# Kernel tuning notes

Hardware: AMD Instinct MI355X
Metric: run time of the kernel (lower is better)

Reference implementation:

```python
import jax, jax.numpy as jnp
import numpy as np

N_NODES = 100000
N_EDGES = 1600000
D_FEAT = 64


def setup_inputs() -> dict:
    key = jax.random.key(0)
    k1, k2, k3 = jax.random.split(key, 3)
    x = jax.random.normal(k1, (N_NODES, D_FEAT), dtype=jnp.float32)
    edge_weight = jax.random.uniform(k2, (N_EDGES,), dtype=jnp.float32)
    edge_index = jax.random.randint(k3, (2, N_EDGES), 0, N_NODES, dtype=jnp.int64)
    return {"x": x, "edge_weight": edge_weight, "edge_index": edge_index}


def reference(x, edge_weight, edge_index):
    # GCNConv with lin.weight forced to identity, improved=False,
    # add_self_loops=True, normalize=True, bias=False.
    N = x.shape[0]
    row, col = edge_index[0], edge_index[1]  # source, target

    # add self loops with fill weight 1.0 (improved=False)
    loop = jnp.arange(N, dtype=edge_index.dtype)
    row = jnp.concatenate([row, loop])
    col = jnp.concatenate([col, loop])
    w = jnp.concatenate([edge_weight, jnp.ones((N,), dtype=x.dtype)])

    # symmetric GCN normalization: deg computed at target (col)
    deg = jax.ops.segment_sum(w, col, num_segments=N)
    deg_inv_sqrt = jnp.where(deg > 0, jax.lax.rsqrt(deg), 0.0)
    norm = deg_inv_sqrt[row] * w * deg_inv_sqrt[col]  # [E+N]

    # gather source features, weight, scatter-add to targets
    msg = x[row] * norm[:, None]                      # [E+N, F]
    out = jax.ops.segment_sum(msg, col, num_segments=N)
    return out
```

## Files before the change

### kernel.cpp

```cpp
#include <hip/hip_runtime.h>

constexpr int N_NODES  = 100000;
constexpr int N_EDGES  = 1600000;
constexpr int D_FEAT   = 64;
constexpr int SCAN_BLK = 1024;
constexpr int NB       = (N_NODES + SCAN_BLK - 1) / SCAN_BLK;

__global__ void k_zero(unsigned long long* __restrict__ packed) {
    int i = blockIdx.x * blockDim.x + threadIdx.x;
    if (i < N_NODES) packed[i] = 0ull;
}

__global__ void k_hist(const float* __restrict__ ew, const int* __restrict__ col,
                       unsigned long long* __restrict__ packed,
                       uchar4* __restrict__ rank4) {
    int t = blockIdx.x * blockDim.x + threadIdx.x;
    if (t >= N_EDGES / 4) return;
    const int4   c4 = ((const int4*)col)[t];
    const float4 w4 = ((const float4*)ew)[t];

    unsigned long long a0 = (1ull << 32) | (unsigned long long)(unsigned int)(w4.x * 16777216.0f + 0.5f);
    unsigned long long a1 = (1ull << 32) | (unsigned long long)(unsigned int)(w4.y * 16777216.0f + 0.5f);
    unsigned long long a2 = (1ull << 32) | (unsigned long long)(unsigned int)(w4.z * 16777216.0f + 0.5f);
    unsigned long long a3 = (1ull << 32) | (unsigned long long)(unsigned int)(w4.w * 16777216.0f + 0.5f);

    unsigned long long o0 = atomicAdd(&packed[c4.x], a0);
    unsigned long long o1 = atomicAdd(&packed[c4.y], a1);
    unsigned long long o2 = atomicAdd(&packed[c4.z], a2);
    unsigned long long o3 = atomicAdd(&packed[c4.w], a3);

    rank4[t] = make_uchar4((unsigned char)(o0 >> 32), (unsigned char)(o1 >> 32),
                           (unsigned char)(o2 >> 32), (unsigned char)(o3 >> 32));
}

__global__ void k_scan_a(const unsigned long long* __restrict__ packed,
                         float* __restrict__ dinv,
                         int* __restrict__ ptr, int* __restrict__ bsum) {
    __shared__ int s[SCAN_BLK];
    int tid = threadIdx.x;
    int gid = blockIdx.x * SCAN_BLK + tid;
    int v = 0;
    if (gid < N_NODES) {
        unsigned long long p = packed[gid];
        v = (int)(p >> 32);
        float deg = (float)(unsigned int)(p & 0xffffffffu) * (1.0f / 16777216.0f);
        dinv[gid] = rsqrtf(deg + 1.0f);
    }
    s[tid] = v;
    __syncthreads();
    for (int off = 1; off < SCAN_BLK; off <<= 1) {
        int t = (tid >= off) ? s[tid - off] : 0;
        __syncthreads();
        s[tid] += t;
        __syncthreads();
    }
    if (gid < N_NODES) ptr[gid] = s[tid] - v;
    if (tid == SCAN_BLK - 1) bsum[blockIdx.x] = s[tid];
}

__global__ void k_scan_b(const int* __restrict__ bsum, int* __restrict__ boff) {
    __shared__ int s[128];
    int tid = threadIdx.x;
    int v = (tid < NB) ? bsum[tid] : 0;
    s[tid] = v;
    __syncthreads();
    for (int off = 1; off < 128; off <<= 1) {
        int t = (tid >= off) ? s[tid - off] : 0;
        __syncthreads();
        s[tid] += t;
        __syncthreads();
    }
    if (tid < NB) boff[tid] = s[tid] - v;
}

__global__ void k_scan_c(const int* __restrict__ boff, int* __restrict__ ptr) {
    int gid = blockIdx.x * SCAN_BLK + threadIdx.x;
    if (gid < N_NODES) ptr[gid] += boff[blockIdx.x];
    if (gid == 0) ptr[N_NODES] = N_EDGES;
}

__global__ void k_scatter(const int* __restrict__ row, const int* __restrict__ col,
                          const float* __restrict__ ew, const float* __restrict__ dinv,
                          const uchar4* __restrict__ rank4,
                          const int* __restrict__ ptr, int2* __restrict__ csr) {
    int t = blockIdx.x * blockDim.x + threadIdx.x;
    if (t >= N_EDGES / 4) return;
    const int4   r4 = ((const int4*)row)[t];
    const int4   c4 = ((const int4*)col)[t];
    const float4 w4 = ((const float4*)ew)[t];
    const uchar4 k4 = rank4[t];

    float d0 = dinv[r4.x], d1 = dinv[r4.y], d2 = dinv[r4.z], d3 = dinv[r4.w];
    int p0 = ptr[c4.x] + k4.x;
    int p1 = ptr[c4.y] + k4.y;
    int p2 = ptr[c4.z] + k4.z;
    int p3 = ptr[c4.w] + k4.w;

    csr[p0] = make_int2(r4.x, __float_as_int(w4.x * d0));
    csr[p1] = make_int2(r4.y, __float_as_int(w4.y * d1));
    csr[p2] = make_int2(r4.z, __float_as_int(w4.z * d2));
    csr[p3] = make_int2(r4.w, __float_as_int(w4.w * d3));
}

__global__ void k_gather(const float* __restrict__ x, const float* __restrict__ dinv,
                         const int* __restrict__ ptr,
                         const int2* __restrict__ csr, float* __restrict__ out) {
    long long gid = (long long)blockIdx.x * blockDim.x + threadIdx.x;
    int node = (int)(gid >> 6);
    if (node >= N_NODES) return;
    int lane = (int)(gid & 63);
    int sub  = lane >> 4;
    int q    = lane & 15;

    int start = ptr[node];
    int n     = ptr[node + 1] - start;

    float4 acc = make_float4(0.f, 0.f, 0.f, 0.f);
    int k = sub;
    for (; k + 4 < n; k += 8) {
        int2 pa = csr[start + k];
        int2 pb = csr[start + k + 4];
        const float4 xa = ((const float4*)(x + (size_t)pa.x * D_FEAT))[q];
        const float4 xb = ((const float4*)(x + (size_t)pb.x * D_FEAT))[q];
        float sa = __int_as_float(pa.y);
        float sb = __int_as_float(pb.y);
        acc.x = fmaf(sa, xa.x, acc.x); acc.y = fmaf(sa, xa.y, acc.y);
        acc.z = fmaf(sa, xa.z, acc.z); acc.w = fmaf(sa, xa.w, acc.w);
        acc.x = fmaf(sb, xb.x, acc.x); acc.y = fmaf(sb, xb.y, acc.y);
        acc.z = fmaf(sb, xb.z, acc.z); acc.w = fmaf(sb, xb.w, acc.w);
    }
    if (k < n) {
        int2 p = csr[start + k];
        const float4 xv = ((const float4*)(x + (size_t)p.x * D_FEAT))[q];
        float s = __int_as_float(p.y);
        acc.x = fmaf(s, xv.x, acc.x); acc.y = fmaf(s, xv.y, acc.y);
        acc.z = fmaf(s, xv.z, acc.z); acc.w = fmaf(s, xv.w, acc.w);
    }

    acc.x += __shfl_xor(acc.x, 16); acc.x += __shfl_xor(acc.x, 32);
    acc.y += __shfl_xor(acc.y, 16); acc.y += __shfl_xor(acc.y, 32);
    acc.z += __shfl_xor(acc.z, 16); acc.z += __shfl_xor(acc.z, 32);
    acc.w += __shfl_xor(acc.w, 16); acc.w += __shfl_xor(acc.w, 32);

    if (sub == 0) {
        float di = dinv[node];
        const float4 xs = ((const float4*)(x + (size_t)node * D_FEAT))[q];
        float4 o;
        o.x = di * acc.x + di * di * xs.x;
        o.y = di * acc.y + di * di * xs.y;
        o.z = di * acc.z + di * di * xs.z;
        o.w = di * acc.w + di * di * xs.w;
        ((float4*)(out + (size_t)node * D_FEAT))[q] = o;
    }
}

extern "C" void kernel_launch(void* const* d_in, const int* in_sizes, int n_in,
                              void* d_out, int out_size, void* d_ws, size_t ws_size,
                              hipStream_t stream) {
    const float* x   = (const float*)d_in[0];
    const float* ew  = (const float*)d_in[1];
    const int*   ei  = (const int*)d_in[2];
    const int*   row = ei;
    const int*   col = ei + N_EDGES;
    float* out = (float*)d_out;

    char* ws = (char*)d_ws;
    unsigned long long* packed = (unsigned long long*)(ws);
    float*         dinv  = (float*)(ws + 800000);
    int*           ptr   = (int*)(ws + 1200000);
    int*           bsum  = (int*)(ws + 1600016);
    int*           boff  = (int*)(ws + 1600528);
    uchar4*        rank4 = (uchar4*)(ws + 1601040);
    int2*          csr   = (int2*)(ws + 3201040);

    const int B = 256;

    k_zero<<<(N_NODES + B - 1) / B, B, 0, stream>>>(packed);
    k_hist<<<(N_EDGES / 4 + B - 1) / B, B, 0, stream>>>(ew, col, packed, rank4);
    k_scan_a<<<NB, SCAN_BLK, 0, stream>>>(packed, dinv, ptr, bsum);
    k_scan_b<<<1, 128, 0, stream>>>(bsum, boff);
    k_scan_c<<<NB, SCAN_BLK, 0, stream>>>(boff, ptr);
    k_scatter<<<(N_EDGES / 4 + B - 1) / B, B, 0, stream>>>(row, col, ew, dinv, rank4, ptr, csr);

    long long total_threads = (long long)N_NODES * 64;
    k_gather<<<(int)((total_threads + B - 1) / B), B, 0, stream>>>(
        x, dinv, ptr, csr, out);
}
```

Before: 251.5 us.

## Gather from fp16 copy of features and fold block-offset scan into add pass

The histogram kernel now also converts x to an fp16 copy, and the gather kernel reads neighbour and self features from that copy, halving the bytes per random row fetch. The separate single-block scan of block sums is removed. Each block of the final pass now reduces the preceding block sums itself with warp shuffles, saving one launch. The risk is fp16 rounding of the features in the output, plus the extra conversion pass over x (read 25.6MB, write 12.8MB) added to the hist kernel.

```diff
diff --git a/kernel.cpp b/kernel.cpp
--- a/kernel.cpp
+++ b/kernel.cpp
@@ -1,4 +1,5 @@
 #include <hip/hip_runtime.h>
+#include <hip/hip_fp16.h>
 
 constexpr int N_NODES  = 100000;
 constexpr int N_EDGES  = 1600000;
@@ -6,31 +7,43 @@
 constexpr int SCAN_BLK = 1024;
 constexpr int NB       = (N_NODES + SCAN_BLK - 1) / SCAN_BLK;
 
+struct alignas(16) Half8 { __half2 h0, h1, h2, h3; };
+struct alignas(8)  Half4 { __half2 h0, h1; };
+
 __global__ void k_zero(unsigned long long* __restrict__ packed) {
     int i = blockIdx.x * blockDim.x + threadIdx.x;
     if (i < N_NODES) packed[i] = 0ull;
 }
 
 __global__ void k_hist(const float* __restrict__ ew, const int* __restrict__ col,
+                       const float* __restrict__ x,
                        unsigned long long* __restrict__ packed,
-                       uchar4* __restrict__ rank4) {
+                       uchar4* __restrict__ rank4, __half* __restrict__ xh) {
     int t = blockIdx.x * blockDim.x + threadIdx.x;
-    if (t >= N_EDGES / 4) return;
-    const int4   c4 = ((const int4*)col)[t];
-    const float4 w4 = ((const float4*)ew)[t];
-
-    unsigned long long a0 = (1ull << 32) | (unsigned long long)(unsigned int)(w4.x * 16777216.0f + 0.5f);
-    unsigned long long a1 = (1ull << 32) | (unsigned long long)(unsigned int)(w4.y * 16777216.0f + 0.5f);
-    unsigned long long a2 = (1ull << 32) | (unsigned long long)(unsigned int)(w4.z * 16777216.0f + 0.5f);
-    unsigned long long a3 = (1ull << 32) | (unsigned long long)(unsigned int)(w4.w * 16777216.0f + 0.5f);
-
-    unsigned long long o0 = atomicAdd(&packed[c4.x], a0);
-    unsigned long long o1 = atomicAdd(&packed[c4.y], a1);
-    unsigned long long o2 = atomicAdd(&packed[c4.z], a2);
-    unsigned long long o3 = atomicAdd(&packed[c4.w], a3);
-
-    rank4[t] = make_uchar4((unsigned char)(o0 >> 32), (unsigned char)(o1 >> 32),
-                           (unsigned char)(o2 >> 32), (unsigned char)(o3 >> 32));
+    if (t < N_EDGES / 4) {
+        const int4   c4 = ((const int4*)col)[t];
+        const float4 w4 = ((const float4*)ew)[t];
+        unsigned long long a0 = (1ull << 32) | (unsigned long long)(unsigned int)(w4.x * 16777216.0f + 0.5f);
+        unsigned long long a1 = (1ull << 32) | (unsigned long long)(unsigned int)(w4.y * 16777216.0f + 0.5f);
+        unsigned long long a2 = (1ull << 32) | (unsigned long long)(unsigned int)(w4.z * 16777216.0f + 0.5f);
+        unsigned long long a3 = (1ull << 32) | (unsigned long long)(unsigned int)(w4.w * 16777216.0f + 0.5f);
+        unsigned long long o0 = atomicAdd(&packed[c4.x], a0);
+        unsigned long long o1 = atomicAdd(&packed[c4.y], a1);
+        unsigned long long o2 = atomicAdd(&packed[c4.z], a2);
+        unsigned long long o3 = atomicAdd(&packed[c4.w], a3);
+        rank4[t] = make_uchar4((unsigned char)(o0 >> 32), (unsigned char)(o1 >> 32),
+                               (unsigned char)(o2 >> 32), (unsigned char)(o3 >> 32));
+    }
+    if (t < N_NODES * D_FEAT / 8) {
+        const float4 f0 = ((const float4*)x)[2 * t];
+        const float4 f1 = ((const float4*)x)[2 * t + 1];
+        Half8 h;
+        h.h0 = __float22half2_rn(make_float2(f0.x, f0.y));
+        h.h1 = __float22half2_rn(make_float2(f0.z, f0.w));
+        h.h2 = __float22half2_rn(make_float2(f1.x, f1.y));
+        h.h3 = __float22half2_rn(make_float2(f1.z, f1.w));
+        ((Half8*)xh)[t] = h;
+    }
 }
 
 __global__ void k_scan_a(const unsigned long long* __restrict__ packed,
@@ -58,24 +71,21 @@
     if (tid == SCAN_BLK - 1) bsum[blockIdx.x] = s[tid];
 }
 
-__global__ void k_scan_b(const int* __restrict__ bsum, int* __restrict__ boff) {
-    __shared__ int s[128];
+__global__ void k_scan_c(const int* __restrict__ bsum, int* __restrict__ ptr) {
+    __shared__ int off_s;
     int tid = threadIdx.x;
-    int v = (tid < NB) ? bsum[tid] : 0;
-    s[tid] = v;
+    if (tid < 64) {
+        int v = 0;
+        if (tid < (int)blockIdx.x) v += bsum[tid];
+        int t2 = tid + 64;
+        if (t2 < (int)blockIdx.x) v += bsum[t2];
+        for (int d = 32; d; d >>= 1) v += __shfl_down(v, d);
+        if (tid == 0) off_s = v;
+    }
     __syncthreads();
-    for (int off = 1; off < 128; off <<= 1) {
-        int t = (tid >= off) ? s[tid - off] : 0;
-        __syncthreads();
-        s[tid] += t;
-        __syncthreads();
-    }
-    if (tid < NB) boff[tid] = s[tid] - v;
-}
-
-__global__ void k_scan_c(const int* __restrict__ boff, int* __restrict__ ptr) {
-    int gid = blockIdx.x * SCAN_BLK + threadIdx.x;
-    if (gid < N_NODES) ptr[gid] += boff[blockIdx.x];
+    int off = off_s;
+    int gid = blockIdx.x * SCAN_BLK + tid;
+    if (gid < N_NODES) ptr[gid] += off;
     if (gid == 0) ptr[N_NODES] = N_EDGES;
 }
 
@@ -102,7 +112,7 @@
     csr[p3] = make_int2(r4.w, __float_as_int(w4.w * d3));
 }
 
-__global__ void k_gather(const float* __restrict__ x, const float* __restrict__ dinv,
+__global__ void k_gather(const __half* __restrict__ xh, const float* __restrict__ dinv,
                          const int* __restrict__ ptr,
                          const int2* __restrict__ csr, float* __restrict__ out) {
     long long gid = (long long)blockIdx.x * blockDim.x + threadIdx.x;
@@ -120,21 +130,24 @@
     for (; k + 4 < n; k += 8) {
         int2 pa = csr[start + k];
         int2 pb = csr[start + k + 4];
-        const float4 xa = ((const float4*)(x + (size_t)pa.x * D_FEAT))[q];
-        const float4 xb = ((const float4*)(x + (size_t)pb.x * D_FEAT))[q];
+        Half4 ha = ((const Half4*)(xh + (size_t)pa.x * D_FEAT))[q];
+        Half4 hb = ((const Half4*)(xh + (size_t)pb.x * D_FEAT))[q];
         float sa = __int_as_float(pa.y);
         float sb = __int_as_float(pb.y);
-        acc.x = fmaf(sa, xa.x, acc.x); acc.y = fmaf(sa, xa.y, acc.y);
-        acc.z = fmaf(sa, xa.z, acc.z); acc.w = fmaf(sa, xa.w, acc.w);
-        acc.x = fmaf(sb, xb.x, acc.x); acc.y = fmaf(sb, xb.y, acc.y);
-        acc.z = fmaf(sb, xb.z, acc.z); acc.w = fmaf(sb, xb.w, acc.w);
+        float2 a0 = __half22float2(ha.h0), a1 = __half22float2(ha.h1);
+        float2 b0 = __half22float2(hb.h0), b1 = __half22float2(hb.h1);
+        acc.x = fmaf(sa, a0.x, acc.x); acc.y = fmaf(sa, a0.y, acc.y);
+        acc.z = fmaf(sa, a1.x, acc.z); acc.w = fmaf(sa, a1.y, acc.w);
+        acc.x = fmaf(sb, b0.x, acc.x); acc.y = fmaf(sb, b0.y, acc.y);
+        acc.z = fmaf(sb, b1.x, acc.z); acc.w = fmaf(sb, b1.y, acc.w);
     }
     if (k < n) {
         int2 p = csr[start + k];
-        const float4 xv = ((const float4*)(x + (size_t)p.x * D_FEAT))[q];
+        Half4 hv = ((const Half4*)(xh + (size_t)p.x * D_FEAT))[q];
         float s = __int_as_float(p.y);
-        acc.x = fmaf(s, xv.x, acc.x); acc.y = fmaf(s, xv.y, acc.y);
-        acc.z = fmaf(s, xv.z, acc.z); acc.w = fmaf(s, xv.w, acc.w);
+        float2 v0 = __half22float2(hv.h0), v1 = __half22float2(hv.h1);
+        acc.x = fmaf(s, v0.x, acc.x); acc.y = fmaf(s, v0.y, acc.y);
+        acc.z = fmaf(s, v1.x, acc.z); acc.w = fmaf(s, v1.y, acc.w);
     }
 
     acc.x += __shfl_xor(acc.x, 16); acc.x += __shfl_xor(acc.x, 32);
@@ -144,12 +157,13 @@
 
     if (sub == 0) {
         float di = dinv[node];
-        const float4 xs = ((const float4*)(x + (size_t)node * D_FEAT))[q];
+        Half4 hs = ((const Half4*)(xh + (size_t)node * D_FEAT))[q];
+        float2 s0 = __half22float2(hs.h0), s1 = __half22float2(hs.h1);
         float4 o;
-        o.x = di * acc.x + di * di * xs.x;
-        o.y = di * acc.y + di * di * xs.y;
-        o.z = di * acc.z + di * di * xs.z;
-        o.w = di * acc.w + di * di * xs.w;
+        o.x = di * acc.x + di * di * s0.x;
+        o.y = di * acc.y + di * di * s0.y;
+        o.z = di * acc.z + di * di * s1.x;
+        o.w = di * acc.w + di * di * s1.y;
         ((float4*)(out + (size_t)node * D_FEAT))[q] = o;
     }
 }
@@ -166,23 +180,22 @@
 
     char* ws = (char*)d_ws;
     unsigned long long* packed = (unsigned long long*)(ws);
-    float*         dinv  = (float*)(ws + 800000);
-    int*           ptr   = (int*)(ws + 1200000);
-    int*           bsum  = (int*)(ws + 1600016);
-    int*           boff  = (int*)(ws + 1600528);
-    uchar4*        rank4 = (uchar4*)(ws + 1601040);
-    int2*          csr   = (int2*)(ws + 3201040);
+    float*   dinv  = (float*)(ws + 800000);
+    int*     ptr   = (int*)(ws + 1200000);
+    int*     bsum  = (int*)(ws + 1600016);
+    uchar4*  rank4 = (uchar4*)(ws + 1600528);
+    __half*  xh    = (__half*)(ws + 3200528);
+    int2*    csr   = (int2*)(ws + 16000528);
 
     const int B = 256;
 
     k_zero<<<(N_NODES + B - 1) / B, B, 0, stream>>>(packed);
-    k_hist<<<(N_EDGES / 4 + B - 1) / B, B, 0, stream>>>(ew, col, packed, rank4);
+    k_hist<<<(N_NODES * D_FEAT / 8 + B - 1) / B, B, 0, stream>>>(ew, col, x, packed, rank4, xh);
     k_scan_a<<<NB, SCAN_BLK, 0, stream>>>(packed, dinv, ptr, bsum);
-    k_scan_b<<<1, 128, 0, stream>>>(bsum, boff);
-    k_scan_c<<<NB, SCAN_BLK, 0, stream>>>(boff, ptr);
+    k_scan_c<<<NB, SCAN_BLK, 0, stream>>>(bsum, ptr);
     k_scatter<<<(N_EDGES / 4 + B - 1) / B, B, 0, stream>>>(row, col, ew, dinv, rank4, ptr, csr);
 
     long long total_threads = (long long)N_NODES * 64;
     k_gather<<<(int)((total_threads + B - 1) / B), B, 0, stream>>>(
-        x, dinv, ptr, csr, out);
-}
+        xh, dinv, ptr, csr, out);
+}
```

Result: no change. 248.6 us (-1.2%).
